# Kernel optimization log

Measured on AMD Instinct MI355X. Metric: run time of the kernel, lower is better.

## Reference

```python
import jax, jax.numpy as jnp
import numpy as np

N_NODES = 200_000   # total nodes in graph
N1 = 81_920         # layer-1 node set (union of sampled 1-hop neighbors)
B = 8_192           # batch of target nodes
S = 10              # neighbor fanout (num_sample=10 in the torch code)
F = 128             # raw feature dim (input_size)
D = 128             # out_size


def setup_inputs() -> dict:
    key = jax.random.key(0)
    ks = jax.random.split(key, 7)
    raw_features = jax.random.normal(ks[0], (N_NODES, F), dtype=jnp.float32)
    # xavier-ish scale for weights [out, 2*in]
    W1 = jax.random.normal(ks[1], (D, 2 * F), dtype=jnp.float32) * (1.0 / np.sqrt(2 * F))
    W2 = jax.random.normal(ks[2], (D, 2 * D), dtype=jnp.float32) * (1.0 / np.sqrt(2 * D))
    self_idx1 = jax.random.randint(ks[3], (N1,), 0, N_NODES)
    neigh_idx1 = jax.random.randint(ks[4], (N1, S), 0, N_NODES)
    self_idx2 = jax.random.randint(ks[5], (B,), 0, N1)
    neigh_idx2 = jax.random.randint(ks[6], (B, S), 0, N1)
    return {
        "raw_features": raw_features,
        "W1": W1,
        "W2": W2,
        "self_idx1": self_idx1,
        "neigh_idx1": neigh_idx1,
        "self_idx2": self_idx2,
        "neigh_idx2": neigh_idx2,
    }


def _sage_layer(self_feats, agg_feats, W):
    # torch: relu(W.mm(cat([self, agg], 1).t()).t()  == relu(cat @ W.T)
    combined = jnp.concatenate([self_feats, agg_feats], axis=1)
    return jax.nn.relu(combined @ W.T)


def reference(raw_features, W1, W2, self_idx1, neigh_idx1, self_idx2, neigh_idx2):
    # Layer 1: MEAN aggregate sampled neighbors from raw features (dense-mask
    # mean in torch == mean over sampled neighbor rows here), then Sage transform.
    agg1 = jnp.mean(raw_features[neigh_idx1], axis=1)          # [N1, F]
    h1 = _sage_layer(raw_features[self_idx1], agg1, W1)        # [N1, D]
    # Layer 2: aggregate over layer-1 embeddings (indices map into layer-1 rows,
    # mirroring _nodes_map / unique_nodes_dict in the torch code).
    agg2 = jnp.mean(h1[neigh_idx2], axis=1)                    # [B, D]
    out = _sage_layer(h1[self_idx2], agg2, W2)                 # [B, D]
    return out
```

## Files before the change

kernel.cpp:

```cpp
#include <hip/hip_runtime.h>
#include <hip/hip_bf16.h>

typedef __attribute__((ext_vector_type(4))) float f32x4;
typedef __attribute__((ext_vector_type(8))) short bf16x8;

__device__ __forceinline__ unsigned short f2bf(float f) {
    unsigned int u = __float_as_uint(f);
    u = (u + 0x7FFFu + ((u >> 16) & 1u)) >> 16;
    return (unsigned short)u;
}

__device__ __forceinline__ float bf2f(unsigned short u) {
    return __uint_as_float(((unsigned int)u) << 16);
}

__global__ __launch_bounds__(256) void cvt_fused(const float* __restrict__ feat,
                                                 const float* __restrict__ W1,
                                                 const float* __restrict__ W2,
                                                 unsigned short* __restrict__ featb,
                                                 unsigned short* __restrict__ W1b,
                                                 unsigned short* __restrict__ W2b) {
    if (blockIdx.x < 12500) {
        size_t i = ((size_t)blockIdx.x * 256 + threadIdx.x) * 8;
        f32x4 a = __builtin_nontemporal_load((const f32x4*)(feat + i));
        f32x4 b = __builtin_nontemporal_load((const f32x4*)(feat + i + 4));
        bf16x8 o;
        o[0] = (short)f2bf(a[0]); o[1] = (short)f2bf(a[1]);
        o[2] = (short)f2bf(a[2]); o[3] = (short)f2bf(a[3]);
        o[4] = (short)f2bf(b[0]); o[5] = (short)f2bf(b[1]);
        o[6] = (short)f2bf(b[2]); o[7] = (short)f2bf(b[3]);
        *(bf16x8*)(featb + i) = o;
    } else {
        int i = (blockIdx.x - 12500) * 256 + threadIdx.x;
        W1b[i] = f2bf(__builtin_nontemporal_load(W1 + i));
        W2b[i] = f2bf(__builtin_nontemporal_load(W2 + i));
    }
}

template<bool OUT_BF16>
__global__ __launch_bounds__(256, 4)
void sage_layer32(const unsigned short* __restrict__ src,
                  const unsigned short* __restrict__ Wb,
                  const int* __restrict__ self_idx,
                  const int* __restrict__ neigh_idx,
                  void* __restrict__ out_v) {
    __shared__ unsigned short As[32][264];
    __shared__ int sIdx[32];
    __shared__ int nIdx[320];

    const int t = threadIdx.x;
    const int rowBase = blockIdx.x * 32;

    if (t < 32) sIdx[t] = self_idx[rowBase + t];
    for (int i = t; i < 320; i += 256) nIdx[i] = neigh_idx[rowBase * 10 + i];
    __syncthreads();

    const int r0 = t >> 4;
    const int r1 = r0 + 16;
    const int co = (t & 15) * 8;

    bf16x8 sv0 = *(const bf16x8*)(src + (size_t)sIdx[r0] * 128 + co);
    bf16x8 sv1 = *(const bf16x8*)(src + (size_t)sIdx[r1] * 128 + co);
    bf16x8 nv0[10], nv1[10];
    #pragma unroll
    for (int sn = 0; sn < 10; ++sn)
        nv0[sn] = *(const bf16x8*)(src + (size_t)nIdx[r0 * 10 + sn] * 128 + co);
    #pragma unroll
    for (int sn = 0; sn < 10; ++sn)
        nv1[sn] = *(const bf16x8*)(src + (size_t)nIdx[r1 * 10 + sn] * 128 + co);

    *(bf16x8*)&As[r0][co] = sv0;
    *(bf16x8*)&As[r1][co] = sv1;

    float s0[8], s1[8];
    #pragma unroll
    for (int e = 0; e < 8; ++e) { s0[e] = 0.f; s1[e] = 0.f; }
    #pragma unroll
    for (int sn = 0; sn < 10; ++sn) {
        #pragma unroll
        for (int e = 0; e < 8; ++e) s0[e] += bf2f((unsigned short)nv0[sn][e]);
    }
    #pragma unroll
    for (int sn = 0; sn < 10; ++sn) {
        #pragma unroll
        for (int e = 0; e < 8; ++e) s1[e] += bf2f((unsigned short)nv1[sn][e]);
    }
    bf16x8 o0, o1;
    #pragma unroll
    for (int e = 0; e < 8; ++e) {
        o0[e] = (short)f2bf(s0[e] * 0.1f);
        o1[e] = (short)f2bf(s1[e] * 0.1f);
    }
    *(bf16x8*)&As[r0][128 + co] = o0;
    *(bf16x8*)&As[r1][128 + co] = o1;
    __syncthreads();

    const int lane = t & 63;
    const int w = t >> 6;
    const int rows16 = (w & 1) * 16;
    const int cols64 = (w >> 1) * 64;
    const int arow = rows16 + (lane & 15);
    const int ko = (lane >> 4) * 8;
    const int ncol = lane & 15;

    f32x4 acc[4];
    #pragma unroll
    for (int i = 0; i < 4; ++i) acc[i] = (f32x4){0.f, 0.f, 0.f, 0.f};

    #pragma unroll
    for (int kk = 0; kk < 8; ++kk) {
        bf16x8 af = *(const bf16x8*)&As[arow][kk * 32 + ko];
        #pragma unroll
        for (int ct = 0; ct < 4; ++ct) {
            const unsigned short* wp = Wb + (size_t)(cols64 + ct * 16 + ncol) * 256 + kk * 32 + ko;
            bf16x8 bf = *(const bf16x8*)wp;
            acc[ct] = __builtin_amdgcn_mfma_f32_16x16x32_bf16(af, bf, acc[ct], 0, 0, 0);
        }
    }

    const int mr = rowBase + rows16 + (lane >> 4) * 4;
    if (OUT_BF16) {
        unsigned short* out = (unsigned short*)out_v;
        #pragma unroll
        for (int ct = 0; ct < 4; ++ct) {
            #pragma unroll
            for (int r = 0; r < 4; ++r) {
                out[(size_t)(mr + r) * 128 + cols64 + ct * 16 + ncol] = f2bf(fmaxf(acc[ct][r], 0.f));
            }
        }
    } else {
        float* out = (float*)out_v;
        #pragma unroll
        for (int ct = 0; ct < 4; ++ct) {
            #pragma unroll
            for (int r = 0; r < 4; ++r) {
                out[(size_t)(mr + r) * 128 + cols64 + ct * 16 + ncol] = fmaxf(acc[ct][r], 0.f);
            }
        }
    }
}

template<bool SRC_BF16, bool OUT_BF16>
__global__ __launch_bounds__(256, 2)
void sage_layer(const void* __restrict__ src_v,
                const unsigned short* __restrict__ Wb,
                const int* __restrict__ self_idx,
                const int* __restrict__ neigh_idx,
                void* __restrict__ out_v) {
    __shared__ unsigned short As[64][264];
    __shared__ int sIdx[64];
    __shared__ int nIdx[64][10];

    const int t = threadIdx.x;
    const int rowBase = blockIdx.x * 64;

    if (t < 64) sIdx[t] = self_idx[rowBase + t];
    for (int i = t; i < 640; i += 256) nIdx[i / 10][i % 10] = neigh_idx[rowBase * 10 + i];
    __syncthreads();

    #pragma unroll
    for (int it = 0; it < 16; ++it) {
        int c = it * 256 + t;
        int row = c >> 6;
        int cc = c & 63;
        float4 v;
        if (cc < 32) {
            if constexpr (SRC_BF16) {
                ushort4 u = *(const ushort4*)((const unsigned short*)src_v + (size_t)sIdx[row] * 128 + cc * 4);
                v.x = bf2f(u.x); v.y = bf2f(u.y); v.z = bf2f(u.z); v.w = bf2f(u.w);
            } else {
                v = *(const float4*)((const float*)src_v + (size_t)sIdx[row] * 128 + cc * 4);
            }
        } else {
            int fo = (cc - 32) * 4;
            float sx = 0.f, sy = 0.f, sz = 0.f, sw = 0.f;
            #pragma unroll
            for (int sn = 0; sn < 10; ++sn) {
                float4 x;
                if constexpr (SRC_BF16) {
                    ushort4 u = *(const ushort4*)((const unsigned short*)src_v + (size_t)nIdx[row][sn] * 128 + fo);
                    x.x = bf2f(u.x); x.y = bf2f(u.y); x.z = bf2f(u.z); x.w = bf2f(u.w);
                } else {
                    x = *(const float4*)((const float*)src_v + (size_t)nIdx[row][sn] * 128 + fo);
                }
                sx += x.x; sy += x.y; sz += x.z; sw += x.w;
            }
            v.x = sx * 0.1f; v.y = sy * 0.1f; v.z = sz * 0.1f; v.w = sw * 0.1f;
        }
        ushort4 o;
        o.x = f2bf(v.x); o.y = f2bf(v.y); o.z = f2bf(v.z); o.w = f2bf(v.w);
        *(ushort4*)&As[row][cc * 4] = o;
    }
    __syncthreads();

    const int lane = t & 63;
    const int w = t >> 6;
    const int arow = w * 16 + (lane & 15);
    const int ko = (lane >> 4) * 8;
    const int ncol = lane & 15;

    f32x4 acc[8];
    #pragma unroll
    for (int i = 0; i < 8; ++i) acc[i] = (f32x4){0.f, 0.f, 0.f, 0.f};

    #pragma unroll
    for (int kk = 0; kk < 8; ++kk) {
        bf16x8 af = *(const bf16x8*)&As[arow][kk * 32 + ko];
        #pragma unroll
        for (int ct = 0; ct < 8; ++ct) {
            const unsigned short* wp = Wb + (ct * 16 + ncol) * 256 + kk * 32 + ko;
            bf16x8 bf = *(const bf16x8*)wp;
            acc[ct] = __builtin_amdgcn_mfma_f32_16x16x32_bf16(af, bf, acc[ct], 0, 0, 0);
        }
    }

    const int mr = rowBase + w * 16 + (lane >> 4) * 4;
    if (OUT_BF16) {
        unsigned short* out = (unsigned short*)out_v;
        #pragma unroll
        for (int ct = 0; ct < 8; ++ct) {
            #pragma unroll
            for (int r = 0; r < 4; ++r) {
                out[(size_t)(mr + r) * 128 + ct * 16 + ncol] = f2bf(fmaxf(acc[ct][r], 0.f));
            }
        }
    } else {
        float* out = (float*)out_v;
        #pragma unroll
        for (int ct = 0; ct < 8; ++ct) {
            #pragma unroll
            for (int r = 0; r < 4; ++r) {
                out[(size_t)(mr + r) * 128 + ct * 16 + ncol] = fmaxf(acc[ct][r], 0.f);
            }
        }
    }
}

extern "C" void kernel_launch(void* const* d_in, const int* in_sizes, int n_in,
                              void* d_out, int out_size, void* d_ws, size_t ws_size,
                              hipStream_t stream) {
    const float* raw   = (const float*)d_in[0];
    const float* W1    = (const float*)d_in[1];
    const float* W2    = (const float*)d_in[2];
    const int* self1   = (const int*)d_in[3];
    const int* neigh1  = (const int*)d_in[4];
    const int* self2   = (const int*)d_in[5];
    const int* neigh2  = (const int*)d_in[6];
    float* out = (float*)d_out;

    char* ws = (char*)d_ws;
    unsigned short* W1b  = (unsigned short*)ws;
    unsigned short* W2b  = W1b + 128 * 256;
    unsigned short* h1   = W2b + 128 * 256;
    unsigned short* rawb = h1 + (size_t)81920 * 128;
    const size_t need = (size_t)(128 * 256 * 2 + 81920 * 128 + (size_t)200000 * 128) * 2;

    cvt_fused<<<12628, 256, 0, stream>>>(raw, W1, W2, rawb, W1b, W2b);

    if (ws_size >= need) {
        sage_layer32<true><<<81920 / 32, 256, 0, stream>>>(
            rawb, W1b, self1, neigh1, (void*)h1);
        sage_layer32<false><<<8192 / 32, 256, 0, stream>>>(
            h1, W2b, self2, neigh2, (void*)out);
    } else {
        sage_layer<false, true><<<81920 / 64, 256, 0, stream>>>(
            (const void*)raw, W1b, self1, neigh1, (void*)h1);
        sage_layer<true, false><<<8192 / 64, 256, 0, stream>>>(
            (const void*)h1, W2b, self2, neigh2, (void*)out);
    }
}
```

Before: 94.34 us.

## Split layer-1 into separate gather-aggregate kernel and dense MFMA GEMM kernel

When the workspace is large enough, layer 1 is split in two. A gather kernel averages neighbour rows and writes the concatenated [self, mean] bf16 rows to a staging buffer, then a GEMM kernel reads that buffer and runs the MFMA matmul with ReLU. This separates the latency-bound gather from the matrix multiply so each kernel can use its own parallelism and occupancy. The cost is an extra write and read of an 81920x256 bf16 buffer (about 80 MB of traffic) and one more launch, and the new path depends on ws_size being large enough.

New measurement: 122.6 us. +29.9%, slower.

```diff
diff --git a/kernel.cpp b/kernel.cpp
--- a/kernel.cpp
+++ b/kernel.cpp
@@ -37,6 +37,119 @@
     }
 }
 
+__global__ void sage_agg(const unsigned short* __restrict__ src,
+                         const int* __restrict__ self_idx,
+                         const int* __restrict__ neigh_idx,
+                         unsigned short* __restrict__ comb) {
+    const int t = threadIdx.x;
+    const int m = blockIdx.x * 16 + (t >> 4);
+    const int co = (t & 15) * 8;
+
+    const int si = self_idx[m];
+    int ni[10];
+    #pragma unroll
+    for (int j = 0; j < 10; ++j) ni[j] = neigh_idx[m * 10 + j];
+
+    bf16x8 sv = *(const bf16x8*)(src + (size_t)si * 128 + co);
+
+    float s[8];
+    #pragma unroll
+    for (int e = 0; e < 8; ++e) s[e] = 0.f;
+
+    {
+        bf16x8 nv[5];
+        #pragma unroll
+        for (int j = 0; j < 5; ++j)
+            nv[j] = *(const bf16x8*)(src + (size_t)ni[j] * 128 + co);
+        #pragma unroll
+        for (int j = 0; j < 5; ++j) {
+            #pragma unroll
+            for (int e = 0; e < 8; ++e) s[e] += bf2f((unsigned short)nv[j][e]);
+        }
+    }
+    {
+        bf16x8 nv[5];
+        #pragma unroll
+        for (int j = 0; j < 5; ++j)
+            nv[j] = *(const bf16x8*)(src + (size_t)ni[5 + j] * 128 + co);
+        #pragma unroll
+        for (int j = 0; j < 5; ++j) {
+            #pragma unroll
+            for (int e = 0; e < 8; ++e) s[e] += bf2f((unsigned short)nv[j][e]);
+        }
+    }
+
+    bf16x8 o;
+    #pragma unroll
+    for (int e = 0; e < 8; ++e) o[e] = (short)f2bf(s[e] * 0.1f);
+
+    unsigned short* cp = comb + (size_t)m * 256;
+    *(bf16x8*)(cp + co) = sv;
+    *(bf16x8*)(cp + 128 + co) = o;
+}
+
+template<bool OUT_BF16>
+__global__ __launch_bounds__(256, 4)
+void sage_gemm(const unsigned short* __restrict__ comb,
+               const unsigned short* __restrict__ Wb,
+               void* __restrict__ out_v) {
+    __shared__ unsigned short As[64][264];
+
+    const int t = threadIdx.x;
+    const int rowBase = blockIdx.x * 64;
+
+    #pragma unroll
+    for (int it = 0; it < 8; ++it) {
+        int i = it * 256 + t;
+        int row = i >> 5, ch = i & 31;
+        bf16x8 v = *(const bf16x8*)(comb + (size_t)(rowBase + row) * 256 + ch * 8);
+        *(bf16x8*)&As[row][ch * 8] = v;
+    }
+    __syncthreads();
+
+    const int lane = t & 63;
+    const int w = t >> 6;
+    const int arow = w * 16 + (lane & 15);
+    const int ko = (lane >> 4) * 8;
+    const int ncol = lane & 15;
+
+    f32x4 acc[8];
+    #pragma unroll
+    for (int i = 0; i < 8; ++i) acc[i] = (f32x4){0.f, 0.f, 0.f, 0.f};
+
+    #pragma unroll
+    for (int kk = 0; kk < 8; ++kk) {
+        bf16x8 af = *(const bf16x8*)&As[arow][kk * 32 + ko];
+        #pragma unroll
+        for (int ct = 0; ct < 8; ++ct) {
+            const unsigned short* wp = Wb + (ct * 16 + ncol) * 256 + kk * 32 + ko;
+            bf16x8 bf = *(const bf16x8*)wp;
+            acc[ct] = __builtin_amdgcn_mfma_f32_16x16x32_bf16(af, bf, acc[ct], 0, 0, 0);
+        }
+    }
+
+    const int mr = rowBase + w * 16 + (lane >> 4) * 4;
+    if (OUT_BF16) {
+        unsigned short* out = (unsigned short*)out_v;
+        #pragma unroll
+        for (int ct = 0; ct < 8; ++ct) {
+            #pragma unroll
+            for (int r = 0; r < 4; ++r) {
+                out[(size_t)(mr + r) * 128 + ct * 16 + ncol] = f2bf(fmaxf(acc[ct][r], 0.f));
+            }
+        }
+    } else {
+        float* out = (float*)out_v;
+        #pragma unroll
+        for (int ct = 0; ct < 8; ++ct) {
+            #pragma unroll
+            for (int r = 0; r < 4; ++r) {
+                out[(size_t)(mr + r) * 128 + ct * 16 + ncol] = fmaxf(acc[ct][r], 0.f);
+            }
+        }
+    }
+}
+
 template<bool OUT_BF16>
 __global__ __launch_bounds__(256, 4)
 void sage_layer32(const unsigned short* __restrict__ src,
@@ -253,11 +366,19 @@
     unsigned short* W2b  = W1b + 128 * 256;
     unsigned short* h1   = W2b + 128 * 256;
     unsigned short* rawb = h1 + (size_t)81920 * 128;
-    const size_t need = (size_t)(128 * 256 * 2 + 81920 * 128 + (size_t)200000 * 128) * 2;
+    unsigned short* comb = rawb + (size_t)200000 * 128;
+
+    const size_t need_mid  = (size_t)(128 * 256 * 2 + 81920 * 128 + (size_t)200000 * 128) * 2;
+    const size_t need_full = need_mid + (size_t)81920 * 256 * 2;
 
     cvt_fused<<<12628, 256, 0, stream>>>(raw, W1, W2, rawb, W1b, W2b);
 
-    if (ws_size >= need) {
+    if (ws_size >= need_full) {
+        sage_agg<<<81920 / 16, 256, 0, stream>>>(rawb, self1, neigh1, comb);
+        sage_gemm<true><<<81920 / 64, 256, 0, stream>>>(comb, W1b, (void*)h1);
+        sage_layer32<false><<<8192 / 32, 256, 0, stream>>>(
+            h1, W2b, self2, neigh2, (void*)out);
+    } else if (ws_size >= need_mid) {
         sage_layer32<true><<<81920 / 32, 256, 0, stream>>>(
             rawb, W1b, self1, neigh1, (void*)h1);
         sage_layer32<false><<<8192 / 32, 256, 0, stream>>>(
```
